# Optimization experiments

Measured on AMD Instinct MI355X. Metric: run time of the kernel, lower is better.

## Reference

```python
import jax, jax.numpy as jnp
import numpy as np
from jax import lax

K_ITERS = 35

def _conv3x3_same(x, w, b):
    # x: [B,1,H,W], w: [1,1,3,3]
    y = lax.conv_general_dilated(x, w, window_strides=(1, 1),
                                 padding=((1, 1), (1, 1)),
                                 dimension_numbers=('NCHW', 'OIHW', 'NCHW'))
    return y + b.reshape(1, -1, 1, 1)

def _maxpool3x3_same(v):
    # 3x3 max pool, stride 1, padding 1 (torch MaxPool2d(kernel=3, stride=1, padding=1))
    return lax.reduce_window(v, -jnp.inf, lax.max,
                             window_dimensions=(1, 1, 3, 3),
                             window_strides=(1, 1, 1, 1),
                             padding=((0, 0), (0, 0), (1, 1), (1, 1)))

def setup_inputs() -> dict:
    key = jax.random.key(0)
    k1, k2, k3 = jax.random.split(key, 3)
    B, H, W = 64, 192, 192
    X = jax.random.uniform(k1, (B, 2, H, W), dtype=jnp.float32)  # grid, goal in [0,1)
    hp_w = jax.random.uniform(k2, (1, 1, 3, 3), dtype=jnp.float32) * 0.5
    p_w = jax.random.uniform(k3, (1, 1, 3, 3), dtype=jnp.float32) * 0.5
    hp_b = jnp.zeros((1,), dtype=jnp.float32)
    p_b = jnp.zeros((1,), dtype=jnp.float32)
    return {"X": X, "hp_w": hp_w, "hp_b": hp_b, "p_w": p_w, "p_b": p_b}

def reference(X, hp_w, hp_b, p_w, p_b):
    grid = X[:, 0:1]           # [B,1,H,W]
    goal = X[:, 1:2]           # [B,1,H,W]
    r = -(1.0 - goal)          # reward map in [-1, 0]
    # process_image: double conv -> wall/flow probability p in (0,1)
    h = jax.nn.relu(_conv3x3_same(grid, hp_w, hp_b))
    p = jax.nn.sigmoid(_conv3x3_same(h, p_w, p_b))
    # value iteration: v = max(v, r + p * (maxpool(v) - r)), k=35 steps
    def body(_, v):
        return jnp.maximum(v, r + p * (_maxpool3x3_same(v) - r))
    v = lax.fori_loop(0, K_ITERS, body, r)
    return (v[:, 0], p[:, 0])  # squeeze channel dim -> ([B,H,W], [B,H,W])
```

## Files before the change

kernel.cpp:

```cpp
#include <hip/hip_runtime.h>

#define HH 192
#define WW 192
#define HW 36864
#define BB 64
#define NPIX 2359296
#define NCH 48
#define NEG (-1.0e30f)

__device__ __forceinline__ float4 conv3x3_chunk(const float* __restrict__ img,
                                                int y, int ch, const float* __restrict__ w9,
                                                float bias) {
  float4 acc = make_float4(bias, bias, bias, bias);
  int x0 = ch * 4;
#pragma unroll
  for (int dy = -1; dy <= 1; ++dy) {
    int yy = y + dy;
    if (yy < 0 || yy >= HH) continue;
    const float* row = img + yy * WW + x0;
    float4 v = *reinterpret_cast<const float4*>(row);
    float l = (ch > 0) ? row[-1] : 0.f;
    float r = (ch < NCH - 1) ? row[4] : 0.f;
    float wa = w9[(dy + 1) * 3 + 0];
    float wb = w9[(dy + 1) * 3 + 1];
    float wc = w9[(dy + 1) * 3 + 2];
    acc.x += wa * l   + wb * v.x + wc * v.y;
    acc.y += wa * v.x + wb * v.y + wc * v.z;
    acc.z += wa * v.y + wb * v.z + wc * v.w;
    acc.w += wa * v.z + wb * v.w + wc * r;
  }
  return acc;
}

__global__ __launch_bounds__(256) void k_conv_h(const float* __restrict__ X,
                                                const float* __restrict__ w9,
                                                const float* __restrict__ b1,
                                                float* __restrict__ h) {
  int idx = blockIdx.x * 256 + threadIdx.x;
  if (idx >= NPIX / 4) return;
  int b = idx / (HW / 4);
  int rem = idx - b * (HW / 4);
  int y = rem / NCH;
  int ch = rem - y * NCH;
  float4 acc = conv3x3_chunk(X + (size_t)b * (2 * HW), y, ch, w9, b1[0]);
  acc.x = fmaxf(acc.x, 0.f); acc.y = fmaxf(acc.y, 0.f);
  acc.z = fmaxf(acc.z, 0.f); acc.w = fmaxf(acc.w, 0.f);
  *reinterpret_cast<float4*>(h + (size_t)b * HW + y * WW + ch * 4) = acc;
}

__global__ __launch_bounds__(256) void k_conv_p(const float* __restrict__ h,
                                                const float* __restrict__ w9,
                                                const float* __restrict__ b1,
                                                float* __restrict__ p_out) {
  int idx = blockIdx.x * 256 + threadIdx.x;
  if (idx >= NPIX / 4) return;
  int b = idx / (HW / 4);
  int rem = idx - b * (HW / 4);
  int y = rem / NCH;
  int ch = rem - y * NCH;
  float4 acc = conv3x3_chunk(h + (size_t)b * HW, y, ch, w9, b1[0]);
  acc.x = 1.f / (1.f + __expf(-acc.x));
  acc.y = 1.f / (1.f + __expf(-acc.y));
  acc.z = 1.f / (1.f + __expf(-acc.z));
  acc.w = 1.f / (1.f + __expf(-acc.w));
  *reinterpret_cast<float4*>(p_out + (size_t)b * HW + y * WW + ch * 4) = acc;
}

template <int FIRST>
__global__ __launch_bounds__(256, 1) void k_span(const float* __restrict__ v_in,
                                                 const float* __restrict__ p_glob,
                                                 const float* __restrict__ X,
                                                 float* __restrict__ v_out) {
  int wid = blockIdx.x * 4 + (threadIdx.x >> 6);
  int lane = threadIdx.x & 63;
  int b = wid >> 4;
  int t = wid & 15;
  int ti = t >> 2, tj = t & 3;
  int ly = lane >> 3, lx = lane & 7;
  int py = ti * 48 - 8 + ly * 8;
  int px = tj * 48 - 8 + lx * 8;
  bool colok = (px >= 0 && px < WW);

  const float* gimg = X + (size_t)b * (2 * HW) + HW;
  const float* pimg = p_glob + (size_t)b * HW;
  const float* vimg = v_in + (size_t)b * HW;

  float v[8][8], p[8][8], c[8][8];
#pragma unroll
  for (int r = 0; r < 8; ++r) {
    int gy = py + r;
    if (colok && gy >= 0 && gy < HH) {
      float4 g0 = *(const float4*)(gimg + gy * WW + px);
      float4 g1 = *(const float4*)(gimg + gy * WW + px + 4);
      float4 p0 = *(const float4*)(pimg + gy * WW + px);
      float4 p1 = *(const float4*)(pimg + gy * WW + px + 4);
      float gg[8] = {g0.x, g0.y, g0.z, g0.w, g1.x, g1.y, g1.z, g1.w};
      float pp[8] = {p0.x, p0.y, p0.z, p0.w, p1.x, p1.y, p1.z, p1.w};
#pragma unroll
      for (int j = 0; j < 8; ++j) {
        p[r][j] = pp[j];
        c[r][j] = (gg[j] - 1.f) * (1.f - pp[j]);
      }
      if (FIRST) {
#pragma unroll
        for (int j = 0; j < 8; ++j) v[r][j] = gg[j] - 1.f;
      } else {
        float4 v0 = *(const float4*)(vimg + gy * WW + px);
        float4 v1 = *(const float4*)(vimg + gy * WW + px + 4);
        v[r][0] = v0.x; v[r][1] = v0.y; v[r][2] = v0.z; v[r][3] = v0.w;
        v[r][4] = v1.x; v[r][5] = v1.y; v[r][6] = v1.z; v[r][7] = v1.w;
      }
    } else {
#pragma unroll
      for (int j = 0; j < 8; ++j) { v[r][j] = NEG; p[r][j] = 0.f; c[r][j] = NEG; }
    }
  }

  int lup = (lane - 8) & 63, ldn = (lane + 8) & 63;
  int llt = (lane - 1) & 63, lrt = (lane + 1) & 63;

#pragma unroll 1
  for (int it = 0; it < 7; ++it) {
    float th[8], bh[8];
#pragma unroll
    for (int j = 0; j < 8; ++j) { float s = __shfl(v[7][j], lup, 64); th[j] = (ly == 0) ? NEG : s; }
#pragma unroll
    for (int j = 0; j < 8; ++j) { float s = __shfl(v[0][j], ldn, 64); bh[j] = (ly == 7) ? NEG : s; }
    float vm[8][8];
#pragma unroll
    for (int r = 0; r < 8; ++r) {
#pragma unroll
      for (int j = 0; j < 8; ++j) {
        float up = (r == 0) ? th[j] : v[r - 1][j];
        float dn = (r == 7) ? bh[j] : v[r + 1][j];
        vm[r][j] = fmaxf(fmaxf(up, dn), v[r][j]);
      }
    }
#pragma unroll
    for (int r = 0; r < 8; ++r) {
      float sl = __shfl(vm[r][7], llt, 64);
      float sr = __shfl(vm[r][0], lrt, 64);
      float lvm = (lx == 0) ? NEG : sl;
      float rvm = (lx == 7) ? NEG : sr;
      float hm0 = fmaxf(lvm, fmaxf(vm[r][0], vm[r][1]));
      float hm7 = fmaxf(vm[r][6], fmaxf(vm[r][7], rvm));
      v[r][0] = fmaxf(v[r][0], fmaf(p[r][0], hm0, c[r][0]));
#pragma unroll
      for (int j = 1; j < 7; ++j) {
        float hm = fmaxf(vm[r][j - 1], fmaxf(vm[r][j], vm[r][j + 1]));
        v[r][j] = fmaxf(v[r][j], fmaf(p[r][j], hm, c[r][j]));
      }
      v[r][7] = fmaxf(v[r][7], fmaf(p[r][7], hm7, c[r][7]));
    }
  }

  if (ly >= 1 && ly <= 6 && lx >= 1 && lx <= 6) {
    float* wimg = v_out + (size_t)b * HW;
#pragma unroll
    for (int r = 0; r < 8; ++r) {
      *(float4*)(wimg + (py + r) * WW + px) = make_float4(v[r][0], v[r][1], v[r][2], v[r][3]);
      *(float4*)(wimg + (py + r) * WW + px + 4) = make_float4(v[r][4], v[r][5], v[r][6], v[r][7]);
    }
  }
}

extern "C" void kernel_launch(void* const* d_in, const int* in_sizes, int n_in,
                              void* d_out, int out_size, void* d_ws, size_t ws_size,
                              hipStream_t stream) {
  const float* X = (const float*)d_in[0];
  const float* hp_w = (const float*)d_in[1];
  const float* hp_b = (const float*)d_in[2];
  const float* p_w = (const float*)d_in[3];
  const float* p_b = (const float*)d_in[4];

  float* out = (float*)d_out;
  float* out_v = out;
  float* out_p = out + NPIX;
  float* bufA = (float*)d_ws;

  float* h = out_v;

  int nblk = (NPIX / 4 + 255) / 256;
  k_conv_h<<<nblk, 256, 0, stream>>>(X, hp_w, hp_b, h);
  k_conv_p<<<nblk, 256, 0, stream>>>(h, p_w, p_b, out_p);

  k_span<1><<<256, 256, 0, stream>>>(X , out_p, X, out_v);
  k_span<0><<<256, 256, 0, stream>>>(out_v, out_p, X, bufA);
  k_span<0><<<256, 256, 0, stream>>>(bufA, out_p, X, out_v);
  k_span<0><<<256, 256, 0, stream>>>(out_v, out_p, X, bufA);
  k_span<0><<<256, 256, 0, stream>>>(bufA, out_p, X, out_v);
}
```

Baseline: 166.4 us.

## Fuse both convolutions and all 35 value iterations into one kernel

Measured after the change: 138.0 us. -17.0%, faster.

```diff
diff --git a/kernel.cpp b/kernel.cpp
--- a/kernel.cpp
+++ b/kernel.cpp
@@ -3,163 +3,158 @@
 #define HH 192
 #define WW 192
 #define HW 36864
-#define BB 64
 #define NPIX 2359296
-#define NCH 48
 #define NEG (-1.0e30f)
+#define RPW 15
+#define HALO 36
 
-__device__ __forceinline__ float4 conv3x3_chunk(const float* __restrict__ img,
-                                                int y, int ch, const float* __restrict__ w9,
-                                                float bias) {
-  float4 acc = make_float4(bias, bias, bias, bias);
-  int x0 = ch * 4;
+__global__ __launch_bounds__(512, 2)
+void k_mvprop(const float* __restrict__ X,
+              const float* __restrict__ hw9p, const float* __restrict__ hbp,
+              const float* __restrict__ pw9p, const float* __restrict__ pbp,
+              float* __restrict__ out_v, float* __restrict__ out_p) {
+  __shared__ float lds_x[2][8][2][WW];
+
+  const int blk = blockIdx.x;
+  const int b = blk >> 2;
+  const int s = blk & 3;
+  const int w = threadIdx.x >> 6;
+  const int lane = threadIdx.x & 63;
+  const int col0 = lane * 3;
+  const int grow0 = s * 48 - HALO + w * RPW;
+
+  const float* gridp = X + (size_t)b * (2 * HW);
+  const float* goalp = gridp + HW;
+
+  float hw[9], pw[9];
 #pragma unroll
-  for (int dy = -1; dy <= 1; ++dy) {
-    int yy = y + dy;
-    if (yy < 0 || yy >= HH) continue;
-    const float* row = img + yy * WW + x0;
-    float4 v = *reinterpret_cast<const float4*>(row);
-    float l = (ch > 0) ? row[-1] : 0.f;
-    float r = (ch < NCH - 1) ? row[4] : 0.f;
-    float wa = w9[(dy + 1) * 3 + 0];
-    float wb = w9[(dy + 1) * 3 + 1];
-    float wc = w9[(dy + 1) * 3 + 2];
-    acc.x += wa * l   + wb * v.x + wc * v.y;
-    acc.y += wa * v.x + wb * v.y + wc * v.z;
-    acc.z += wa * v.y + wb * v.z + wc * v.w;
-    acc.w += wa * v.z + wb * v.w + wc * r;
-  }
-  return acc;
-}
+  for (int i = 0; i < 9; ++i) { hw[i] = hw9p[i]; pw[i] = pw9p[i]; }
+  const float hb = hbp[0], pb = pbp[0];
 
-__global__ __launch_bounds__(256) void k_conv_h(const float* __restrict__ X,
-                                                const float* __restrict__ w9,
-                                                const float* __restrict__ b1,
-                                                float* __restrict__ h) {
-  int idx = blockIdx.x * 256 + threadIdx.x;
-  if (idx >= NPIX / 4) return;
-  int b = idx / (HW / 4);
-  int rem = idx - b * (HW / 4);
-  int y = rem / NCH;
-  int ch = rem - y * NCH;
-  float4 acc = conv3x3_chunk(X + (size_t)b * (2 * HW), y, ch, w9, b1[0]);
-  acc.x = fmaxf(acc.x, 0.f); acc.y = fmaxf(acc.y, 0.f);
-  acc.z = fmaxf(acc.z, 0.f); acc.w = fmaxf(acc.w, 0.f);
-  *reinterpret_cast<float4*>(h + (size_t)b * HW + y * WW + ch * 4) = acc;
-}
-
-__global__ __launch_bounds__(256) void k_conv_p(const float* __restrict__ h,
-                                                const float* __restrict__ w9,
-                                                const float* __restrict__ b1,
-                                                float* __restrict__ p_out) {
-  int idx = blockIdx.x * 256 + threadIdx.x;
-  if (idx >= NPIX / 4) return;
-  int b = idx / (HW / 4);
-  int rem = idx - b * (HW / 4);
-  int y = rem / NCH;
-  int ch = rem - y * NCH;
-  float4 acc = conv3x3_chunk(h + (size_t)b * HW, y, ch, w9, b1[0]);
-  acc.x = 1.f / (1.f + __expf(-acc.x));
-  acc.y = 1.f / (1.f + __expf(-acc.y));
-  acc.z = 1.f / (1.f + __expf(-acc.z));
-  acc.w = 1.f / (1.f + __expf(-acc.w));
-  *reinterpret_cast<float4*>(p_out + (size_t)b * HW + y * WW + ch * 4) = acc;
-}
-
-template <int FIRST>
-__global__ __launch_bounds__(256, 1) void k_span(const float* __restrict__ v_in,
-                                                 const float* __restrict__ p_glob,
-                                                 const float* __restrict__ X,
-                                                 float* __restrict__ v_out) {
-  int wid = blockIdx.x * 4 + (threadIdx.x >> 6);
-  int lane = threadIdx.x & 63;
-  int b = wid >> 4;
-  int t = wid & 15;
-  int ti = t >> 2, tj = t & 3;
-  int ly = lane >> 3, lx = lane & 7;
-  int py = ti * 48 - 8 + ly * 8;
-  int px = tj * 48 - 8 + lx * 8;
-  bool colok = (px >= 0 && px < WW);
-
-  const float* gimg = X + (size_t)b * (2 * HW) + HW;
-  const float* pimg = p_glob + (size_t)b * HW;
-  const float* vimg = v_in + (size_t)b * HW;
-
-  float v[8][8], p[8][8], c[8][8];
+  float v_[RPW][3], p_[RPW][3], c_[RPW][3];
+  {
+    float ga[7], gb2[7], gc[7], ha[5], hb2[5], hc[5];
 #pragma unroll
-  for (int r = 0; r < 8; ++r) {
-    int gy = py + r;
-    if (colok && gy >= 0 && gy < HH) {
-      float4 g0 = *(const float4*)(gimg + gy * WW + px);
-      float4 g1 = *(const float4*)(gimg + gy * WW + px + 4);
-      float4 p0 = *(const float4*)(pimg + gy * WW + px);
-      float4 p1 = *(const float4*)(pimg + gy * WW + px + 4);
-      float gg[8] = {g0.x, g0.y, g0.z, g0.w, g1.x, g1.y, g1.z, g1.w};
-      float pp[8] = {p0.x, p0.y, p0.z, p0.w, p1.x, p1.y, p1.z, p1.w};
+    for (int j = 0; j < 7; ++j) { ga[j] = gb2[j] = gc[j] = 0.f; }
 #pragma unroll
-      for (int j = 0; j < 8; ++j) {
-        p[r][j] = pp[j];
-        c[r][j] = (gg[j] - 1.f) * (1.f - pp[j]);
+    for (int j = 0; j < 5; ++j) { ha[j] = hb2[j] = hc[j] = 0.f; }
+#pragma unroll
+    for (int t = 0; t < RPW + 4; ++t) {
+      int grow = grow0 - 2 + t;
+#pragma unroll
+      for (int j = 0; j < 7; ++j) { ga[j] = gb2[j]; gb2[j] = gc[j]; }
+      if (grow >= 0 && grow < HH) {
+        const float* rp = gridp + grow * WW;
+#pragma unroll
+        for (int j = 0; j < 7; ++j) {
+          int cc = col0 - 2 + j;
+          gc[j] = (cc >= 0 && cc < WW) ? rp[cc] : 0.f;
+        }
+      } else {
+#pragma unroll
+        for (int j = 0; j < 7; ++j) gc[j] = 0.f;
       }
-      if (FIRST) {
+      if (t >= 2) {
+        int hrow = grow0 - 3 + t;
+        bool hrok = (hrow >= 0 && hrow < HH);
 #pragma unroll
-        for (int j = 0; j < 8; ++j) v[r][j] = gg[j] - 1.f;
-      } else {
-        float4 v0 = *(const float4*)(vimg + gy * WW + px);
-        float4 v1 = *(const float4*)(vimg + gy * WW + px + 4);
-        v[r][0] = v0.x; v[r][1] = v0.y; v[r][2] = v0.z; v[r][3] = v0.w;
-        v[r][4] = v1.x; v[r][5] = v1.y; v[r][6] = v1.z; v[r][7] = v1.w;
+        for (int j = 0; j < 5; ++j) { ha[j] = hb2[j]; hb2[j] = hc[j]; }
+#pragma unroll
+        for (int j = 0; j < 5; ++j) {
+          int hcol = col0 - 1 + j;
+          float acc = hb;
+#pragma unroll
+          for (int dj = 0; dj < 3; ++dj) {
+            acc = fmaf(ga[j + dj], hw[0 + dj], acc);
+            acc = fmaf(gb2[j + dj], hw[3 + dj], acc);
+            acc = fmaf(gc[j + dj], hw[6 + dj], acc);
+          }
+          hc[j] = (hrok && hcol >= 0 && hcol < WW) ? fmaxf(acc, 0.f) : 0.f;
+        }
       }
-    } else {
+      if (t >= 4) {
+        int r = t - 4;
+        int prow = grow0 + r;
+        if (prow >= 0 && prow < HH) {
+          const float* glr = goalp + prow * WW;
 #pragma unroll
-      for (int j = 0; j < 8; ++j) { v[r][j] = NEG; p[r][j] = 0.f; c[r][j] = NEG; }
+          for (int j = 0; j < 3; ++j) {
+            float z = pb;
+#pragma unroll
+            for (int dj = 0; dj < 3; ++dj) {
+              z = fmaf(ha[j + dj], pw[0 + dj], z);
+              z = fmaf(hb2[j + dj], pw[3 + dj], z);
+              z = fmaf(hc[j + dj], pw[6 + dj], z);
+            }
+            float pv = 1.f / (1.f + __expf(-z));
+            float gl = glr[col0 + j];
+            p_[r][j] = pv;
+            v_[r][j] = gl - 1.f;
+            c_[r][j] = (gl - 1.f) * (1.f - pv);
+          }
+        } else {
+#pragma unroll
+          for (int j = 0; j < 3; ++j) { p_[r][j] = 0.f; v_[r][j] = NEG; c_[r][j] = NEG; }
+        }
+      }
     }
   }
 
-  int lup = (lane - 8) & 63, ldn = (lane + 8) & 63;
-  int llt = (lane - 1) & 63, lrt = (lane + 1) & 63;
+  const int llt = (lane - 1) & 63, lrt = (lane + 1) & 63;
+  int par = 0;
 
 #pragma unroll 1
-  for (int it = 0; it < 7; ++it) {
-    float th[8], bh[8];
+  for (int it = 0; it < 35; ++it) {
 #pragma unroll
-    for (int j = 0; j < 8; ++j) { float s = __shfl(v[7][j], lup, 64); th[j] = (ly == 0) ? NEG : s; }
+    for (int j = 0; j < 3; ++j) {
+      lds_x[par][w][0][col0 + j] = v_[0][j];
+      lds_x[par][w][1][col0 + j] = v_[RPW - 1][j];
+    }
+    __syncthreads();
+    float vt0 = (w > 0) ? lds_x[par][w - 1][1][col0 + 0] : NEG;
+    float vt1 = (w > 0) ? lds_x[par][w - 1][1][col0 + 1] : NEG;
+    float vt2 = (w > 0) ? lds_x[par][w - 1][1][col0 + 2] : NEG;
+    float vb0 = (w < 7) ? lds_x[par][w + 1][0][col0 + 0] : NEG;
+    float vb1 = (w < 7) ? lds_x[par][w + 1][0][col0 + 1] : NEG;
+    float vb2 = (w < 7) ? lds_x[par][w + 1][0][col0 + 2] : NEG;
+    par ^= 1;
+
+    float pr0 = vt0, pr1 = vt1, pr2 = vt2;
 #pragma unroll
-    for (int j = 0; j < 8; ++j) { float s = __shfl(v[0][j], ldn, 64); bh[j] = (ly == 7) ? NEG : s; }
-    float vm[8][8];
-#pragma unroll
-    for (int r = 0; r < 8; ++r) {
-#pragma unroll
-      for (int j = 0; j < 8; ++j) {
-        float up = (r == 0) ? th[j] : v[r - 1][j];
-        float dn = (r == 7) ? bh[j] : v[r + 1][j];
-        vm[r][j] = fmaxf(fmaxf(up, dn), v[r][j]);
-      }
-    }
-#pragma unroll
-    for (int r = 0; r < 8; ++r) {
-      float sl = __shfl(vm[r][7], llt, 64);
-      float sr = __shfl(vm[r][0], lrt, 64);
-      float lvm = (lx == 0) ? NEG : sl;
-      float rvm = (lx == 7) ? NEG : sr;
-      float hm0 = fmaxf(lvm, fmaxf(vm[r][0], vm[r][1]));
-      float hm7 = fmaxf(vm[r][6], fmaxf(vm[r][7], rvm));
-      v[r][0] = fmaxf(v[r][0], fmaf(p[r][0], hm0, c[r][0]));
-#pragma unroll
-      for (int j = 1; j < 7; ++j) {
-        float hm = fmaxf(vm[r][j - 1], fmaxf(vm[r][j], vm[r][j + 1]));
-        v[r][j] = fmaxf(v[r][j], fmaf(p[r][j], hm, c[r][j]));
-      }
-      v[r][7] = fmaxf(v[r][7], fmaf(p[r][7], hm7, c[r][7]));
+    for (int r = 0; r < RPW; ++r) {
+      float nx0 = (r < RPW - 1) ? v_[r + 1][0] : vb0;
+      float nx1 = (r < RPW - 1) ? v_[r + 1][1] : vb1;
+      float nx2 = (r < RPW - 1) ? v_[r + 1][2] : vb2;
+      float vm0 = fmaxf(fmaxf(pr0, v_[r][0]), nx0);
+      float vm1 = fmaxf(fmaxf(pr1, v_[r][1]), nx1);
+      float vm2 = fmaxf(fmaxf(pr2, v_[r][2]), nx2);
+      float lvm = __shfl(vm2, llt, 64);
+      float rvm = __shfl(vm0, lrt, 64);
+      if (lane == 0) lvm = NEG;
+      if (lane == 63) rvm = NEG;
+      float hm0 = fmaxf(lvm, fmaxf(vm0, vm1));
+      float hm1 = fmaxf(vm0, fmaxf(vm1, vm2));
+      float hm2 = fmaxf(vm1, fmaxf(vm2, rvm));
+      float o0 = v_[r][0], o1 = v_[r][1], o2 = v_[r][2];
+      v_[r][0] = fmaxf(o0, fmaf(p_[r][0], hm0, c_[r][0]));
+      v_[r][1] = fmaxf(o1, fmaf(p_[r][1], hm1, c_[r][1]));
+      v_[r][2] = fmaxf(o2, fmaf(p_[r][2], hm2, c_[r][2]));
+      pr0 = o0; pr1 = o1; pr2 = o2;
     }
   }
 
-  if (ly >= 1 && ly <= 6 && lx >= 1 && lx <= 6) {
-    float* wimg = v_out + (size_t)b * HW;
+  const int cr0 = s * 48, cr1 = s * 48 + 48;
+  float* vout = out_v + (size_t)b * HW;
+  float* pout = out_p + (size_t)b * HW;
 #pragma unroll
-    for (int r = 0; r < 8; ++r) {
-      *(float4*)(wimg + (py + r) * WW + px) = make_float4(v[r][0], v[r][1], v[r][2], v[r][3]);
-      *(float4*)(wimg + (py + r) * WW + px + 4) = make_float4(v[r][4], v[r][5], v[r][6], v[r][7]);
+  for (int r = 0; r < RPW; ++r) {
+    int grow = grow0 + r;
+    if (grow >= cr0 && grow < cr1) {
+#pragma unroll
+      for (int j = 0; j < 3; ++j) {
+        vout[grow * WW + col0 + j] = v_[r][j];
+        pout[grow * WW + col0 + j] = p_[r][j];
+      }
     }
   }
 }
@@ -176,17 +171,6 @@
   float* out = (float*)d_out;
   float* out_v = out;
   float* out_p = out + NPIX;
-  float* bufA = (float*)d_ws;
 
-  float* h = out_v;
-
-  int nblk = (NPIX / 4 + 255) / 256;
-  k_conv_h<<<nblk, 256, 0, stream>>>(X, hp_w, hp_b, h);
-  k_conv_p<<<nblk, 256, 0, stream>>>(h, p_w, p_b, out_p);
-
-  k_span<1><<<256, 256, 0, stream>>>(X , out_p, X, out_v);
-  k_span<0><<<256, 256, 0, stream>>>(out_v, out_p, X, bufA);
-  k_span<0><<<256, 256, 0, stream>>>(bufA, out_p, X, out_v);
-  k_span<0><<<256, 256, 0, stream>>>(out_v, out_p, X, bufA);
-  k_span<0><<<256, 256, 0, stream>>>(bufA, out_p, X, out_v);
+  k_mvprop<<<256, 512, 0, stream>>>(X, hp_w, hp_b, p_w, p_b, out_v, out_p);
 }
```
